# Optimization experiments

Hardware: AMD Instinct MI355X
Metric: run time of the kernel (lower is better)

The kernel has to match this reference:

```python
import jax, jax.numpy as jnp
import numpy as np

B, N, SU, H, NC, NUM_ITER = 1024, 32, 8, 64, 4, 5
E = N * (N - 1)


def _edge_idx(n):
    # Fully-connected graph without self loops; edges grouped contiguously by
    # destination node so that blocks of (n-1) messages sum into one node
    # (matches the original Python segment-sum loop with step = n-1).
    idx = np.arange(n)
    temp_a = np.concatenate([np.delete(idx, j) for j in range(n)])  # sources
    temp_b = np.repeat(idx, n - 1)                                   # destinations
    return temp_a, temp_b


def _lin(x, W, b):
    return x @ W.T + b


def setup_inputs():
    key = jax.random.key(0)
    ks = jax.random.split(key, 20)
    f = jax.random.normal
    return {
        "read_gru": f(ks[0], (B, N, SU), jnp.float32),
        "gru_init": f(ks[1], (B, N, H), jnp.float32),
        "init_features": f(ks[2], (B, N, 3), jnp.float32),
        "edge_weight": f(ks[3], (B, E), jnp.float32),
        "noise_info": jax.random.uniform(ks[4], (B, 1), jnp.float32),
        "x_hat_EP": f(ks[5], (B, N), jnp.float32),
        "variance_EP": jax.random.uniform(ks[6], (B, N), jnp.float32),
        "W1a": f(ks[7], (SU, 3)) * 0.3, "b1a": jnp.zeros((SU,)),
        "W2a": f(ks[8], (H, 2 * SU + 2)) * 0.1, "b2a": jnp.zeros((H,)),
        "W2b": f(ks[9], (H // 2, H)) * 0.1, "b2b": jnp.zeros((H // 2,)),
        "W2c": f(ks[10], (SU, H // 2)) * 0.1, "b2c": jnp.zeros((SU,)),
        "Wih": f(ks[11], (3 * H, SU + 2)) * 0.1, "bih": jnp.zeros((3 * H,)),
        "Whh": f(ks[12], (3 * H, H)) * 0.1, "bhh": jnp.zeros((3 * H,)),
        "W3a": f(ks[13], (H, SU)) * 0.1, "b3a": jnp.zeros((H,)),
        "W3b": f(ks[14], (H // 2, H)) * 0.1, "b3b": jnp.zeros((H // 2,)),
        "W3c": f(ks[15], (NC, H // 2)) * 0.1, "b3c": jnp.zeros((NC,)),
        "W4": f(ks[16], (SU, H)) * 0.1, "b4": jnp.zeros((SU,)),
        "GNN_iter": 0,
    }


def reference(read_gru, gru_init, init_features, edge_weight, noise_info,
              x_hat_EP, variance_EP,
              W1a, b1a, W2a, b2a, W2b, b2b, W2c, b2c,
              Wih, bih, Whh, bhh,
              W3a, b3a, W3b, b3b, W3c, b3c, W4, b4, GNN_iter):
    b, n = init_features.shape[0], init_features.shape[1]
    temp_a, temp_b = _edge_idx(n)
    e = temp_a.shape[0]
    edge_e = edge_weight[:, :, None]                              # [B,E,1]
    noise_e = jnp.broadcast_to(noise_info, (b, e))[:, :, None]    # [B,E,1]
    gru_hidden = gru_init
    for it in range(NUM_ITER):
        if it == 0 and GNN_iter == 0:
            init_nodes = _lin(init_features, W1a, b1a)            # [B,N,SU]
        else:
            init_nodes = read_gru
        s1 = init_nodes[:, temp_a, :]                             # gather sources
        s2 = init_nodes[:, temp_b, :]                             # gather dests
        comb = jnp.concatenate([s1, s2, edge_e, noise_e], axis=2) # [B,E,2SU+2]
        m = jax.nn.relu(_lin(comb, W2a, b2a))
        m = jax.nn.relu(_lin(m, W2b, b2b))
        m = jax.nn.relu(_lin(m, W2c, b2c))                        # [B,E,SU]
        # contiguous blocks of (n-1) messages per destination node
        sum_msgs = m.reshape(b, n, n - 1, -1).sum(axis=2)         # [B,N,SU]
        gin = jnp.concatenate(
            [sum_msgs, x_hat_EP[:, :, None], variance_EP[:, :, None]], axis=2)
        # GRUCell applied per node
        gi = _lin(gin, Wih, bih)
        gh = _lin(gru_hidden, Whh, bhh)
        i_r, i_z, i_n = jnp.split(gi, 3, axis=-1)
        h_r, h_z, h_n = jnp.split(gh, 3, axis=-1)
        r = jax.nn.sigmoid(i_r + h_r)
        z = jax.nn.sigmoid(i_z + h_z)
        cand = jnp.tanh(i_n + r * h_n)
        gru_hidden = (1.0 - z) * cand + z * gru_hidden
        read_gru = _lin(gru_hidden, W4, b4)
    # readout (no activations in original forward)
    p_y_x = _lin(_lin(_lin(read_gru, W3a, b3a), W3b, b3b), W3c, b3c)
    return (p_y_x, read_gru, gru_hidden)
```

## Files before the change

### kernel.cpp

```cpp
#include <hip/hip_runtime.h>
#include <hip/hip_bf16.h>

#define BB 1024
#define NN 32
#define SUD 8
#define HD 64
#define NCD 4
#define ED 992
#define NITER 5

#define O_W2AT 0
#define O_B2A  1152
#define O_W2B  1216
#define O_B2B  3264
#define O_W2CT 3296
#define O_B2C  3552
#define O_WIHT 3560
#define O_BIH  5480
#define O_WHHT 5672
#define O_BHH  17960
#define O_W4T  18152
#define O_B4   18664
#define O_W3AT 18672
#define O_B3A  19184
#define O_W3BT 19248
#define O_B3B  21296
#define O_W3CT 21328
#define O_B3C  21456
#define O_W1AT 21460
#define O_B1A  21484
#define W_TOTAL 21492
#define O_WIHP 21492
#define W_TOTAL2 25332

#define FRAG_B2   0
#define FRAG_C    2048
#define FRAG_WHH  2560
#define FRAG_A2P  14848
#define FRAG_TOTAL 18944
#define PREP_TOTAL (W_TOTAL2 + FRAG_TOTAL)

#define GHS 196

typedef const float* fwp;
typedef __attribute__((ext_vector_type(8))) short short8;
typedef __attribute__((ext_vector_type(4))) float float4v;
typedef __attribute__((ext_vector_type(2))) float float2v;

__device__ __forceinline__ short bf16r(float x) {
  __hip_bfloat16 h = __float2bfloat16(x);
  return __builtin_bit_cast(short, h);
}
__device__ __forceinline__ float2v mk2(float a, float b) {
  float2v r; r.x = a; r.y = b; return r;
}

__global__ void prep_weights(fwp W2a, fwp b2a, fwp W2b, fwp b2b, fwp W2c, fwp b2c,
                             fwp Wih, fwp bih, fwp Whh, fwp bhh,
                             fwp W3a, fwp b3a, fwp W3b, fwp b3b, fwp W3c, fwp b3c,
                             fwp W4, fwp b4, fwp W1a, fwp b1a, float* __restrict__ ws) {
  int idx = blockIdx.x * 256 + threadIdx.x;
  if (idx >= PREP_TOTAL) return;
  if (idx >= W_TOTAL2) {
    __hip_bfloat16* wbw = (__hip_bfloat16*)(ws + W_TOTAL2);
    int e = idx - W_TOTAL2;
    float v;
    if (e < 2048) {
      int j = e & 7, L = (e >> 3) & 63, hs = e >> 9;
      int h = hs >> 1, s = hs & 1;
      v = W2b[(2 * (L & 15) + h) * 64 + s * 32 + ((L >> 4) & 3) * 8 + j];
    } else if (e < 2560) {
      int e2 = e - 2048;
      int j = e2 & 7, L = (e2 >> 3) & 63;
      int su = L & 15, q = L >> 4;
      v = (su < 8) ? W2c[su * 32 + q * 8 + j] : 0.f;
    } else if (e < 14848) {
      int e2 = e - 2560;
      int j = e2 & 7, L = (e2 >> 3) & 63, nts = e2 >> 9;
      int nt = nts >> 1, s = nts & 1;
      v = Whh[(nt * 16 + (L & 15)) * 64 + s * 32 + ((L >> 4) & 3) * 8 + j];
    } else {
      int e2 = e - 14848;
      int j = e2 & 7, L = (e2 >> 3) & 63, nt = e2 >> 9;
      int col = L & 15, kq = L >> 4;
      v = 0.f;
      if (kq == 0) v = (nt < 4) ? W2a[(nt * 16 + col) * 18 + j]
                                : W2a[((nt - 4) * 16 + col) * 18 + 8 + j];
    }
    wbw[e] = __float2bfloat16(v);
    return;
  }
  if (idx >= W_TOTAL) {
    int p = idx - O_WIHP;
    int o = p / 20, k = (p % 20) >> 1;
    ws[idx] = Wih[o * 10 + k];
    return;
  }
  float v;
  if (idx < O_B2A)       { int p = idx;          int su = p / 64, f = p % 64;   v = W2a[f * 18 + su]; }
  else if (idx < O_W2B)  { v = b2a[idx - O_B2A]; }
  else if (idx < O_B2B)  { v = W2b[idx - O_W2B]; }
  else if (idx < O_W2CT) { v = b2b[idx - O_B2B]; }
  else if (idx < O_B2C)  { int p = idx - O_W2CT; int o = p / 8, su = p % 8;     v = W2c[su * 32 + o]; }
  else if (idx < O_WIHT) { v = b2c[idx - O_B2C]; }
  else if (idx < O_BIH)  { int p = idx - O_WIHT; int k = p / 192, o = p % 192;  v = Wih[o * 10 + k]; }
  else if (idx < O_WHHT) { v = bih[idx - O_BIH]; }
  else if (idx < O_BHH)  { int p = idx - O_WHHT; int k = p / 192, o = p % 192;  v = Whh[o * 64 + k]; }
  else if (idx < O_W4T)  { v = bhh[idx - O_BHH]; }
  else if (idx < O_B4)   { int p = idx - O_W4T;  int k = p / 8, su = p % 8;     v = W4[su * 64 + k]; }
  else if (idx < O_W3AT) { v = b4[idx - O_B4]; }
  else if (idx < O_B3A)  { int p = idx - O_W3AT; int k = p / 64, f = p % 64;    v = W3a[f * 8 + k]; }
  else if (idx < O_W3BT) { v = b3a[idx - O_B3A]; }
  else if (idx < O_B3B)  { int p = idx - O_W3BT; int k = p / 32, f = p % 32;    v = W3b[f * 64 + k]; }
  else if (idx < O_W3CT) { v = b3b[idx - O_B3B]; }
  else if (idx < O_B3C)  { int p = idx - O_W3CT; int k = p / 4, c = p % 4;      v = W3c[c * 32 + k]; }
  else if (idx < O_W1AT) { v = b3c[idx - O_B3C]; }
  else if (idx < O_B1A)  { int p = idx - O_W1AT; int c = p / 8, su = p % 8;     v = W1a[su * 3 + c]; }
  else                   { v = b1a[idx - O_B1A]; }
  ws[idx] = v;
}

#define DO_STEP2(AROW, EWV, KOFF, Y0, Y1, W0, W1, FH0, FH1, ACC0, ACC1)        \
  {                                                                            \
    float4v x0 = *(const float4v*)&sA1[(AROW) * 68 + (KOFF)];                  \
    float4v x1 = *(const float4v*)&sA1[(AROW) * 68 + (KOFF) + 4];              \
    float4v z4 = {0.f, 0.f, 0.f, 0.f};                                         \
    float4v t0 = (x0 + Y0) + (EWV) * W0;                                       \
    float4v t1 = (x1 + Y1) + (EWV) * W1;                                       \
    t0 = __builtin_elementwise_max(t0, z4);                                    \
    t1 = __builtin_elementwise_max(t1, z4);                                    \
    short8 ahi;                                                                \
    ahi[0] = bf16r(t0.x); ahi[1] = bf16r(t0.y); ahi[2] = bf16r(t0.z);          \
    ahi[3] = bf16r(t0.w); ahi[4] = bf16r(t1.x); ahi[5] = bf16r(t1.y);          \
    ahi[6] = bf16r(t1.z); ahi[7] = bf16r(t1.w);                                \
    ACC0 = __builtin_amdgcn_mfma_f32_16x16x32_bf16(ahi, FH0, ACC0, 0, 0, 0);   \
    ACC1 = __builtin_amdgcn_mfma_f32_16x16x32_bf16(ahi, FH1, ACC1, 0, 0, 0);   \
  }

#define LAUNDER(v) __asm__ __volatile__("" : "+v"(v))

__global__ __launch_bounds__(256, 4) void gnn_fused(
    const float* __restrict__ read_gru_in,
    const float* __restrict__ gru_init,
    const float* __restrict__ feat,
    const float* __restrict__ edge_w,
    const float* __restrict__ noise_in,
    const float* __restrict__ xhat,
    const float* __restrict__ vep,
    const int* __restrict__ gnn_iter_p,
    const float* __restrict__ ws,
    const float* __restrict__ W4g,
    float* __restrict__ out)
{
  __shared__ __attribute__((aligned(16))) char spool[NN * GHS * 4];
  __shared__ __attribute__((aligned(16))) float sH[NN * 68];
  __shared__ float sNodes[NN * 9];
  __shared__ float sSum[NN * 8];
  __shared__ float sEw[ED];
  __shared__ float sC1[64];
  __shared__ float sWew[64];
  __shared__ float sX[NN];
  __shared__ float sV[NN];

  float* const sA1 = (float*)spool;
  float* const sA2 = (float*)(spool + 8704);
  __hip_bfloat16* const sM2 = (__hip_bfloat16*)(spool + 17408);
  float* const sGH = (float*)spool;

  const int b = blockIdx.x;
  const int t = threadIdx.x;
  const int lane = t & 63;
  const int wv = t >> 6;
  const int quad = lane >> 4;
  const int lm = lane & 15;

  const __hip_bfloat16* wb = (const __hip_bfloat16*)(ws + W_TOTAL2);

  float noi = noise_in[b];
  for (int e = t; e < ED; e += 256) sEw[e] = edge_w[b * ED + e];
  if (t < NN) { sX[t] = xhat[b * NN + t]; sV[t] = vep[b * NN + t]; }
  if (t < 64) {
    sC1[t]  = ws[O_B2A + t] + noi * ws[O_W2AT + 17 * 64 + t];
    sWew[t] = ws[O_W2AT + 16 * 64 + t];
  }
#pragma unroll
  for (int i = 0; i < 8; ++i) {
    int p = t + 256 * i;
    sH[(p >> 6) * 68 + (p & 63)] = gru_init[b * (NN * HD) + p];
  }
  {
    const int git = gnn_iter_p[0];
    int n = t >> 3, su = t & 7;
    float acc;
    if (git == 0) {
      acc = ws[O_B1A + su];
#pragma unroll
      for (int c = 0; c < 3; ++c)
        acc += ws[O_W1AT + c * 8 + su] * feat[b * (NN * 3) + n * 3 + c];
    } else {
      acc = read_gru_in[b * (NN * SUD) + t];
    }
    sNodes[n * 9 + su] = acc;
  }
  __syncthreads();

  for (int it = 0; it < NITER; ++it) {
    int ive = 0; LAUNDER(ive);
    const float* wsle = ws + ive;
    const __hip_bfloat16* wble = wb + ive;
    short8 fbh00 = *(const short8*)(wble + FRAG_B2 + (0 * 64 + lane) * 8);
    short8 fbh01 = *(const short8*)(wble + FRAG_B2 + (1 * 64 + lane) * 8);
    short8 fbh10 = *(const short8*)(wble + FRAG_B2 + (2 * 64 + lane) * 8);
    short8 fbh11 = *(const short8*)(wble + FRAG_B2 + (3 * 64 + lane) * 8);
    short8 fcf   = *(const short8*)(wble + FRAG_C + lane * 8);
    const float2v b2bv = *(const float2v*)&wsle[O_B2B + 2 * lm];
    const float   b2cl = wsle[O_B2C + lm];

    {
      int iva = 0; LAUNDER(iva);
      const __hip_bfloat16* fp = wb + FRAG_A2P + iva;
      short8 aN[2];
#pragma unroll
      for (int mt = 0; mt < 2; ++mt) {
        short8 a = {0, 0, 0, 0, 0, 0, 0, 0};
        if (quad == 0) {
          const float* np = &sNodes[(mt * 16 + lm) * 9];
#pragma unroll
          for (int q = 0; q < 8; ++q) a[q] = bf16r(np[q]);
        }
        aN[mt] = a;
      }
      const int f = wv * 16 + lm;
      const float c1f = sC1[f];
#pragma unroll
      for (int half = 0; half < 2; ++half) {
        short8 bfr = *(const short8*)(fp + ((half * 4 + wv) * 64 + lane) * 8);
#pragma unroll
        for (int mt = 0; mt < 2; ++mt) {
          float4v acc = {0.f, 0.f, 0.f, 0.f};
          acc = __builtin_amdgcn_mfma_f32_16x16x32_bf16(aN[mt], bfr, acc, 0, 0, 0);
#pragma unroll
          for (int r = 0; r < 4; ++r) {
            int node = mt * 16 + quad * 4 + r;
            if (half == 0) sA1[node * 68 + f] = acc[r];
            else           sA2[node * 68 + f] = acc[r] + c1f;
          }
        }
      }
    }
    __syncthreads();

    {
      int ivz = 0; LAUNDER(ivz);
      __hip_bfloat16* m2w = sM2 + wv * (16 * 44);
      const int kq0 = quad * 8, kq1 = 32 + quad * 8;
      float4v wwA = *(const float4v*)&sWew[ivz + kq0];
      float4v wwB = *(const float4v*)&sWew[ivz + kq0 + 4];
      float4v wwC = *(const float4v*)&sWew[ivz + kq1];
      float4v wwD = *(const float4v*)&sWew[ivz + kq1 + 4];
      const float4v binit0 = {b2bv.x, b2bv.x, b2bv.x, b2bv.x};
      const float4v binit1 = {b2bv.y, b2bv.y, b2bv.y, b2bv.y};
      const float4v cinit  = {b2cl, b2cl, b2cl, b2cl};
      const int kkB = 16 + lm;
      const int kkB2 = (kkB < 31) ? kkB : 0;
      for (int ni = 0; ni < 8; ++ni) {
        const int jj = wv * 8 + ni;
        const int a0 = lm + (lm >= jj ? 1 : 0);
        const int a1 = kkB2 + (kkB2 >= jj ? 1 : 0);
        const float ew0 = sEw[ivz + jj * 31 + lm];
        const float ew1 = (kkB < 31) ? sEw[ivz + jj * 31 + kkB] : 0.f;
        float4v yA = *(const float4v*)&sA2[jj * 68 + kq0];
        float4v yB = *(const float4v*)&sA2[jj * 68 + kq0 + 4];
        float4v yC = *(const float4v*)&sA2[jj * 68 + kq1];
        float4v yD = *(const float4v*)&sA2[jj * 68 + kq1 + 4];
        float4v acc00 = binit0;
        float4v acc01 = binit1;
        DO_STEP2(a0, ew0, kq0, yA, yB, wwA, wwB, fbh00, fbh10, acc00, acc01);
        DO_STEP2(a0, ew0, kq1, yC, yD, wwC, wwD, fbh01, fbh11, acc00, acc01);
#pragma unroll
        for (int r = 0; r < 4; ++r) {
          float m20 = fmaxf(acc00[r], 0.f);
          float m21 = fmaxf(acc01[r], 0.f);
          ushort2 pp;
          pp.x = (unsigned short)bf16r(m20);
          pp.y = (unsigned short)bf16r(m21);
          *(ushort2*)(m2w + (quad * 4 + r) * 44 + 2 * lm) = pp;
        }
        float4v acc10 = binit0;
        float4v acc11 = binit1;
        DO_STEP2(a1, ew1, kq0, yA, yB, wwA, wwB, fbh00, fbh10, acc10, acc11);
        DO_STEP2(a1, ew1, kq1, yC, yD, wwC, wwD, fbh01, fbh11, acc10, acc11);
        __asm__ __volatile__("" ::: "memory");
        float psum;
        {
          short8 ac = *(const short8*)(m2w + lm * 44 + quad * 8);
          float4v c3 = cinit;
          c3 = __builtin_amdgcn_mfma_f32_16x16x32_bf16(ac, fcf, c3, 0, 0, 0);
          psum  = fmaxf(c3[0], 0.f);
          psum += fmaxf(c3[1], 0.f);
          psum += fmaxf(c3[2], 0.f);
          psum += fmaxf(c3[3], 0.f);
        }
        __asm__ __volatile__("" ::: "memory");
#pragma unroll
        for (int r = 0; r < 4; ++r) {
          float m20 = fmaxf(acc10[r], 0.f);
          float m21 = fmaxf(acc11[r], 0.f);
          ushort2 pp;
          pp.x = (unsigned short)bf16r(m20);
          pp.y = (unsigned short)bf16r(m21);
          *(ushort2*)(m2w + (quad * 4 + r) * 44 + 2 * lm) = pp;
        }
        __asm__ __volatile__("" ::: "memory");
        {
          short8 ac = *(const short8*)(m2w + lm * 44 + quad * 8);
          float4v c3 = cinit;
          c3 = __builtin_amdgcn_mfma_f32_16x16x32_bf16(ac, fcf, c3, 0, 0, 0);
#pragma unroll
          for (int r = 0; r < 4; ++r) {
            float v = fmaxf(c3[r], 0.f);
            if (r == 3) v = (quad == 3) ? 0.f : v;
            psum += v;
          }
        }
        __asm__ __volatile__("" ::: "memory");
        psum += __shfl_xor(psum, 16);
        psum += __shfl_xor(psum, 32);
        if (lane < 8) sSum[jj * 8 + lane] = psum;
      }
    }
    __syncthreads();

    {
      int ivg = 0; LAUNDER(ivg);
      const __hip_bfloat16* wbl = wb + ivg;
      short8 aH[2][2];
#pragma unroll
      for (int mt = 0; mt < 2; ++mt) {
#pragma unroll
        for (int s = 0; s < 2; ++s) {
          const float* hp = &sH[(mt * 16 + lm) * 68 + s * 32 + quad * 8];
          float4v h0 = *(const float4v*)hp;
          float4v h1 = *(const float4v*)(hp + 4);
          short8 a;
          a[0] = bf16r(h0.x); a[1] = bf16r(h0.y); a[2] = bf16r(h0.z); a[3] = bf16r(h0.w);
          a[4] = bf16r(h1.x); a[5] = bf16r(h1.y); a[6] = bf16r(h1.z); a[7] = bf16r(h1.w);
          aH[mt][s] = a;
        }
      }
#pragma unroll
      for (int nt = 0; nt < 3; ++nt) {
        int gnt = 4 * nt + wv;
        short8 bh0 = *(const short8*)(wbl + FRAG_WHH + ((gnt * 2 + 0) * 64 + lane) * 8);
        short8 bh1 = *(const short8*)(wbl + FRAG_WHH + ((gnt * 2 + 1) * 64 + lane) * 8);
#pragma unroll
        for (int mt = 0; mt < 2; ++mt) {
          float4v acc = {0.f, 0.f, 0.f, 0.f};
          acc = __builtin_amdgcn_mfma_f32_16x16x32_bf16(aH[mt][0], bh0, acc, 0, 0, 0);
          acc = __builtin_amdgcn_mfma_f32_16x16x32_bf16(aH[mt][1], bh1, acc, 0, 0, 0);
#pragma unroll
          for (int r = 0; r < 4; ++r)
            sGH[(mt * 16 + quad * 4 + r) * GHS + gnt * 16 + lm] = acc[r];
        }
      }
    }
    __asm__ __volatile__("" ::: "memory");

    {
      int ivq = 0; LAUNDER(ivq);
      const float* wsl = ws + ivq;
      int lm2 = lane & 15, g = lane >> 4;
      int c = wv * 16 + lm2;
      const float* wih = wsl + O_WIHP;
      float br = wsl[O_BIH + c]       + wsl[O_BHH + c];
      float bz = wsl[O_BIH + 64 + c]  + wsl[O_BHH + 64 + c];
      float bn = wsl[O_BIH + 128 + c];
      float2v ar2[4], az2[4], an2[4];
#pragma unroll
      for (int jp = 0; jp < 4; ++jp) {
        ar2[jp] = mk2(br, br); az2[jp] = mk2(bz, bz); an2[jp] = mk2(bn, bn);
      }
#pragma unroll
      for (int k = 0; k < 10; ++k) {
        float2v wr = *(const float2v*)&wih[(c) * 20 + 2 * k];
        float2v wz = *(const float2v*)&wih[(64 + c) * 20 + 2 * k];
        float2v wn = *(const float2v*)&wih[(128 + c) * 20 + 2 * k];
#pragma unroll
        for (int jp = 0; jp < 4; ++jp) {
          float2v gg;
          if (k < 8)       gg = mk2(sSum[(g + 8 * jp) * 8 + k], sSum[(g + 8 * jp + 4) * 8 + k]);
          else if (k == 8) gg = mk2(sX[g + 8 * jp], sX[g + 8 * jp + 4]);
          else             gg = mk2(sV[g + 8 * jp], sV[g + 8 * jp + 4]);
          ar2[jp] += wr * gg;
          az2[jp] += wz * gg;
          an2[jp] += wn * gg;
        }
      }
      float bnh = wsl[O_BHH + 128 + c];
      float hnew[8];
#pragma unroll
      for (int j = 0; j < 8; ++j) {
        int n = g + 4 * j;
        int jp = j >> 1;
        float arj = (j & 1) ? ar2[jp].y : ar2[jp].x;
        float azj = (j & 1) ? az2[jp].y : az2[jp].x;
        float anj = (j & 1) ? an2[jp].y : an2[jp].x;
        float ghr = sGH[n * GHS + c];
        float ghz = sGH[n * GHS + 64 + c];
        float ghn = sGH[n * GHS + 128 + c] + bnh;
        float er = __expf(-(arj + ghr));
        float r = __builtin_amdgcn_rcpf(1.f + er);
        float ez = __expf(-(azj + ghz));
        float z = __builtin_amdgcn_rcpf(1.f + ez);
        float cd = anj + r * ghn;
        float e2 = __expf(2.f * cd);
        float th = 1.f - 2.f * __builtin_amdgcn_rcpf(e2 + 1.f);
        float hv = sH[n * 68 + c];
        hnew[j] = th + z * (hv - th);
      }
      __syncthreads();
#pragma unroll
      for (int j = 0; j < 8; ++j) sH[(g + 4 * j) * 68 + c] = hnew[j];
    }
    __syncthreads();

    {
      int ivw = 0; LAUNDER(ivw);
      int n = t >> 3, su = t & 7;
      const float* w4r = W4g + ivw + su * 64;
      float4v acc4 = {0.f, 0.f, 0.f, 0.f};
#pragma unroll
      for (int k = 0; k < 64; k += 4) {
        float4v w = *(const float4v*)&w4r[k];
        float4v h = *(const float4v*)&sH[n * 68 + k];
        acc4 += w * h;
      }
      sNodes[n * 9 + su] = ws[O_B4 + su] + ((acc4.x + acc4.y) + (acc4.z + acc4.w));
    }
    __syncthreads();
  }

#pragma unroll
  for (int i = 0; i < 8; ++i) {
    int p = t + 256 * i;
    int n = p >> 6, f = p & 63;
    float acc = ws[O_B3A + f];
#pragma unroll
    for (int k = 0; k < 8; ++k) acc += ws[O_W3AT + k * 64 + f] * sNodes[n * 9 + k];
    sA1[n * 68 + f] = acc;
  }
  __syncthreads();
#pragma unroll
  for (int i = 0; i < 4; ++i) {
    int p = t + 256 * i;
    int n = p >> 5, f = p & 31;
    float c0 = 0.f, c1v = 0.f, c2 = 0.f, c3v = 0.f;
#pragma unroll
    for (int k = 0; k < 64; k += 4) {
      c0  += ws[O_W3BT + (k + 0) * 32 + f] * sA1[n * 68 + k + 0];
      c1v += ws[O_W3BT + (k + 1) * 32 + f] * sA1[n * 68 + k + 1];
      c2  += ws[O_W3BT + (k + 2) * 32 + f] * sA1[n * 68 + k + 2];
      c3v += ws[O_W3BT + (k + 3) * 32 + f] * sA1[n * 68 + k + 3];
    }
    sA2[n * 33 + f] = ws[O_B3B + f] + ((c0 + c1v) + (c2 + c3v));
  }
  __syncthreads();
  if (t < 128) {
    int n = t >> 2, c = t & 3;
    float acc = ws[O_B3C + c];
#pragma unroll
    for (int k = 0; k < 32; ++k) acc += ws[O_W3CT + k * 4 + c] * sA2[n * 33 + k];
    out[b * (NN * NCD) + t] = acc;
  }
  out[BB * NN * NCD + b * (NN * SUD) + t] = sNodes[(t >> 3) * 9 + (t & 7)];
#pragma unroll
  for (int i = 0; i < 8; ++i) {
    int p = t + 256 * i;
    out[BB * NN * NCD + BB * NN * SUD + b * (NN * HD) + p] =
        sH[(p >> 6) * 68 + (p & 63)];
  }
}

extern "C" void kernel_launch(void* const* d_in, const int* in_sizes, int n_in,
                              void* d_out, int out_size, void* d_ws, size_t ws_size,
                              hipStream_t stream) {
  typedef const float* F32;
  F32 read_gru = (F32)d_in[0];
  F32 gru_init = (F32)d_in[1];
  F32 feat     = (F32)d_in[2];
  F32 edge_w   = (F32)d_in[3];
  F32 noise    = (F32)d_in[4];
  F32 xh       = (F32)d_in[5];
  F32 vp       = (F32)d_in[6];
  F32 W1a = (F32)d_in[7];  F32 b1a = (F32)d_in[8];
  F32 W2a = (F32)d_in[9];  F32 b2a = (F32)d_in[10];
  F32 W2b = (F32)d_in[11]; F32 b2b = (F32)d_in[12];
  F32 W2c = (F32)d_in[13]; F32 b2c = (F32)d_in[14];
  F32 Wih = (F32)d_in[15]; F32 bih = (F32)d_in[16];
  F32 Whh = (F32)d_in[17]; F32 bhh = (F32)d_in[18];
  F32 W3a = (F32)d_in[19]; F32 b3a = (F32)d_in[20];
  F32 W3b = (F32)d_in[21]; F32 b3b = (F32)d_in[22];
  F32 W3c = (F32)d_in[23]; F32 b3c = (F32)d_in[24];
  F32 W4  = (F32)d_in[25]; F32 b4  = (F32)d_in[26];
  const int* git = (const int*)d_in[27];
  float* ws = (float*)d_ws;

  prep_weights<<<(PREP_TOTAL + 255) / 256, 256, 0, stream>>>(
      W2a, b2a, W2b, b2b, W2c, b2c, Wih, bih, Whh, bhh,
      W3a, b3a, W3b, b3b, W3c, b3c, W4, b4, W1a, b1a, ws);

  gnn_fused<<<BB, 256, 0, stream>>>(read_gru, gru_init, feat, edge_w, noise,
                                    xh, vp, git, ws, W4, (float*)d_out);
}
```

Measured before the change: 253.0 us.

## Fuse GRU input projection into MFMA and compute gates directly from accumulators

The GRU input-to-hidden product (summed messages, x_hat, variance against Wih) is now done with bf16 MFMA, using a new zero-padded bf16 fragment layout of Wih packed by the prep kernel. The gate nonlinearities are then applied directly to the MFMA accumulator registers, so the shared-memory round trip through the sGH buffer and its fp32 scalar FMA loop are removed. The r/z/n column split across waves is rearranged so each wave owns matching gate columns. In exchange, the input projection runs at bf16 precision instead of fp32, and the shared-memory pool is resized.

```diff
diff --git a/kernel.cpp b/kernel.cpp
--- a/kernel.cpp
+++ b/kernel.cpp
@@ -40,8 +40,6 @@
 #define FRAG_TOTAL 18944
 #define PREP_TOTAL (W_TOTAL2 + FRAG_TOTAL)
 
-#define GHS 196
-
 typedef const float* fwp;
 typedef __attribute__((ext_vector_type(8))) short short8;
 typedef __attribute__((ext_vector_type(4))) float float4v;
@@ -50,9 +48,6 @@
 __device__ __forceinline__ short bf16r(float x) {
   __hip_bfloat16 h = __float2bfloat16(x);
   return __builtin_bit_cast(short, h);
-}
-__device__ __forceinline__ float2v mk2(float a, float b) {
-  float2v r; r.x = a; r.y = b; return r;
 }
 
 __global__ void prep_weights(fwp W2a, fwp b2a, fwp W2b, fwp b2b, fwp W2c, fwp b2c,
@@ -105,7 +100,24 @@
   else if (idx < O_WIHT) { v = b2c[idx - O_B2C]; }
   else if (idx < O_BIH)  { int p = idx - O_WIHT; int k = p / 192, o = p % 192;  v = Wih[o * 10 + k]; }
   else if (idx < O_WHHT) { v = bih[idx - O_BIH]; }
-  else if (idx < O_BHH)  { int p = idx - O_WHHT; int k = p / 192, o = p % 192;  v = Whh[o * 64 + k]; }
+  else if (idx < O_BHH)  {
+    int p = idx - O_WHHT;
+    if (p < 3072) {
+      unsigned packed = 0;
+#pragma unroll
+      for (int h = 0; h < 2; ++h) {
+        int e = 2 * p + h;
+        int j = e & 7, L = (e >> 3) & 63, nt = e >> 9;
+        int k = ((L >> 4) & 3) * 8 + j;
+        float vv = (k < 10) ? Wih[(nt * 16 + (L & 15)) * 10 + k] : 0.f;
+        unsigned us = (unsigned short)bf16r(vv);
+        packed |= us << (16 * h);
+      }
+      ws[idx] = __builtin_bit_cast(float, packed);
+      return;
+    }
+    int k = p / 192, o = p % 192;  v = Whh[o * 64 + k];
+  }
   else if (idx < O_W4T)  { v = bhh[idx - O_BHH]; }
   else if (idx < O_B4)   { int p = idx - O_W4T;  int k = p / 8, su = p % 8;     v = W4[su * 64 + k]; }
   else if (idx < O_W3AT) { v = b4[idx - O_B4]; }
@@ -152,7 +164,7 @@
     const float* __restrict__ W4g,
     float* __restrict__ out)
 {
-  __shared__ __attribute__((aligned(16))) char spool[NN * GHS * 4];
+  __shared__ __attribute__((aligned(16))) char spool[23040];
   __shared__ __attribute__((aligned(16))) float sH[NN * 68];
   __shared__ float sNodes[NN * 9];
   __shared__ float sSum[NN * 8];
@@ -165,7 +177,6 @@
   float* const sA1 = (float*)spool;
   float* const sA2 = (float*)(spool + 8704);
   __hip_bfloat16* const sM2 = (__hip_bfloat16*)(spool + 17408);
-  float* const sGH = (float*)spool;
 
   const int b = blockIdx.x;
   const int t = threadIdx.x;
@@ -334,7 +345,9 @@
     {
       int ivg = 0; LAUNDER(ivg);
       const __hip_bfloat16* wbl = wb + ivg;
+      const __hip_bfloat16* wihf = (const __hip_bfloat16*)(ws + O_WHHT) + ivg;
       short8 aH[2][2];
+      short8 aG[2];
 #pragma unroll
       for (int mt = 0; mt < 2; ++mt) {
 #pragma unroll
@@ -347,80 +360,90 @@
           a[4] = bf16r(h1.x); a[5] = bf16r(h1.y); a[6] = bf16r(h1.z); a[7] = bf16r(h1.w);
           aH[mt][s] = a;
         }
-      }
-#pragma unroll
-      for (int nt = 0; nt < 3; ++nt) {
-        int gnt = 4 * nt + wv;
+        short8 g = {0, 0, 0, 0, 0, 0, 0, 0};
+        int nrow = mt * 16 + lm;
+        if (quad == 0) {
+          float4v s0 = *(const float4v*)&sSum[nrow * 8];
+          float4v s1 = *(const float4v*)&sSum[nrow * 8 + 4];
+          g[0] = bf16r(s0.x); g[1] = bf16r(s0.y); g[2] = bf16r(s0.z); g[3] = bf16r(s0.w);
+          g[4] = bf16r(s1.x); g[5] = bf16r(s1.y); g[6] = bf16r(s1.z); g[7] = bf16r(s1.w);
+        } else if (quad == 1) {
+          g[0] = bf16r(sX[nrow]);
+          g[1] = bf16r(sV[nrow]);
+        }
+        aG[mt] = g;
+      }
+      const float4v zz4 = {0.f, 0.f, 0.f, 0.f};
+      float4v pr0, pr1, pz0, pz1, phn0, phn1, pin0, pin1;
+      {
+        int gnt = wv;
         short8 bh0 = *(const short8*)(wbl + FRAG_WHH + ((gnt * 2 + 0) * 64 + lane) * 8);
         short8 bh1 = *(const short8*)(wbl + FRAG_WHH + ((gnt * 2 + 1) * 64 + lane) * 8);
-#pragma unroll
-        for (int mt = 0; mt < 2; ++mt) {
-          float4v acc = {0.f, 0.f, 0.f, 0.f};
-          acc = __builtin_amdgcn_mfma_f32_16x16x32_bf16(aH[mt][0], bh0, acc, 0, 0, 0);
-          acc = __builtin_amdgcn_mfma_f32_16x16x32_bf16(aH[mt][1], bh1, acc, 0, 0, 0);
-#pragma unroll
-          for (int r = 0; r < 4; ++r)
-            sGH[(mt * 16 + quad * 4 + r) * GHS + gnt * 16 + lm] = acc[r];
-        }
-      }
-    }
-    __asm__ __volatile__("" ::: "memory");
-
-    {
-      int ivq = 0; LAUNDER(ivq);
-      const float* wsl = ws + ivq;
-      int lm2 = lane & 15, g = lane >> 4;
-      int c = wv * 16 + lm2;
-      const float* wih = wsl + O_WIHP;
-      float br = wsl[O_BIH + c]       + wsl[O_BHH + c];
-      float bz = wsl[O_BIH + 64 + c]  + wsl[O_BHH + 64 + c];
-      float bn = wsl[O_BIH + 128 + c];
-      float2v ar2[4], az2[4], an2[4];
-#pragma unroll
-      for (int jp = 0; jp < 4; ++jp) {
-        ar2[jp] = mk2(br, br); az2[jp] = mk2(bz, bz); an2[jp] = mk2(bn, bn);
-      }
-#pragma unroll
-      for (int k = 0; k < 10; ++k) {
-        float2v wr = *(const float2v*)&wih[(c) * 20 + 2 * k];
-        float2v wz = *(const float2v*)&wih[(64 + c) * 20 + 2 * k];
-        float2v wn = *(const float2v*)&wih[(128 + c) * 20 + 2 * k];
-#pragma unroll
-        for (int jp = 0; jp < 4; ++jp) {
-          float2v gg;
-          if (k < 8)       gg = mk2(sSum[(g + 8 * jp) * 8 + k], sSum[(g + 8 * jp + 4) * 8 + k]);
-          else if (k == 8) gg = mk2(sX[g + 8 * jp], sX[g + 8 * jp + 4]);
-          else             gg = mk2(sV[g + 8 * jp], sV[g + 8 * jp + 4]);
-          ar2[jp] += wr * gg;
-          az2[jp] += wz * gg;
-          an2[jp] += wn * gg;
-        }
-      }
-      float bnh = wsl[O_BHH + 128 + c];
-      float hnew[8];
-#pragma unroll
-      for (int j = 0; j < 8; ++j) {
-        int n = g + 4 * j;
-        int jp = j >> 1;
-        float arj = (j & 1) ? ar2[jp].y : ar2[jp].x;
-        float azj = (j & 1) ? az2[jp].y : az2[jp].x;
-        float anj = (j & 1) ? an2[jp].y : an2[jp].x;
-        float ghr = sGH[n * GHS + c];
-        float ghz = sGH[n * GHS + 64 + c];
-        float ghn = sGH[n * GHS + 128 + c] + bnh;
-        float er = __expf(-(arj + ghr));
-        float r = __builtin_amdgcn_rcpf(1.f + er);
-        float ez = __expf(-(azj + ghz));
-        float z = __builtin_amdgcn_rcpf(1.f + ez);
-        float cd = anj + r * ghn;
-        float e2 = __expf(2.f * cd);
-        float th = 1.f - 2.f * __builtin_amdgcn_rcpf(e2 + 1.f);
-        float hv = sH[n * 68 + c];
-        hnew[j] = th + z * (hv - th);
+        short8 bwi = *(const short8*)(wihf + (gnt * 64 + lane) * 8);
+        pr0 = __builtin_amdgcn_mfma_f32_16x16x32_bf16(aG[0], bwi, zz4, 0, 0, 0);
+        pr0 = __builtin_amdgcn_mfma_f32_16x16x32_bf16(aH[0][0], bh0, pr0, 0, 0, 0);
+        pr0 = __builtin_amdgcn_mfma_f32_16x16x32_bf16(aH[0][1], bh1, pr0, 0, 0, 0);
+        pr1 = __builtin_amdgcn_mfma_f32_16x16x32_bf16(aG[1], bwi, zz4, 0, 0, 0);
+        pr1 = __builtin_amdgcn_mfma_f32_16x16x32_bf16(aH[1][0], bh0, pr1, 0, 0, 0);
+        pr1 = __builtin_amdgcn_mfma_f32_16x16x32_bf16(aH[1][1], bh1, pr1, 0, 0, 0);
+      }
+      {
+        int gnt = 4 + wv;
+        short8 bh0 = *(const short8*)(wbl + FRAG_WHH + ((gnt * 2 + 0) * 64 + lane) * 8);
+        short8 bh1 = *(const short8*)(wbl + FRAG_WHH + ((gnt * 2 + 1) * 64 + lane) * 8);
+        short8 bwi = *(const short8*)(wihf + (gnt * 64 + lane) * 8);
+        pz0 = __builtin_amdgcn_mfma_f32_16x16x32_bf16(aG[0], bwi, zz4, 0, 0, 0);
+        pz0 = __builtin_amdgcn_mfma_f32_16x16x32_bf16(aH[0][0], bh0, pz0, 0, 0, 0);
+        pz0 = __builtin_amdgcn_mfma_f32_16x16x32_bf16(aH[0][1], bh1, pz0, 0, 0, 0);
+        pz1 = __builtin_amdgcn_mfma_f32_16x16x32_bf16(aG[1], bwi, zz4, 0, 0, 0);
+        pz1 = __builtin_amdgcn_mfma_f32_16x16x32_bf16(aH[1][0], bh0, pz1, 0, 0, 0);
+        pz1 = __builtin_amdgcn_mfma_f32_16x16x32_bf16(aH[1][1], bh1, pz1, 0, 0, 0);
+      }
+      {
+        int gnt = 8 + wv;
+        short8 bh0 = *(const short8*)(wbl + FRAG_WHH + ((gnt * 2 + 0) * 64 + lane) * 8);
+        short8 bh1 = *(const short8*)(wbl + FRAG_WHH + ((gnt * 2 + 1) * 64 + lane) * 8);
+        short8 bwi = *(const short8*)(wihf + (gnt * 64 + lane) * 8);
+        phn0 = __builtin_amdgcn_mfma_f32_16x16x32_bf16(aH[0][0], bh0, zz4, 0, 0, 0);
+        phn0 = __builtin_amdgcn_mfma_f32_16x16x32_bf16(aH[0][1], bh1, phn0, 0, 0, 0);
+        phn1 = __builtin_amdgcn_mfma_f32_16x16x32_bf16(aH[1][0], bh0, zz4, 0, 0, 0);
+        phn1 = __builtin_amdgcn_mfma_f32_16x16x32_bf16(aH[1][1], bh1, phn1, 0, 0, 0);
+        pin0 = __builtin_amdgcn_mfma_f32_16x16x32_bf16(aG[0], bwi, zz4, 0, 0, 0);
+        pin1 = __builtin_amdgcn_mfma_f32_16x16x32_bf16(aG[1], bwi, zz4, 0, 0, 0);
+      }
+      const int c = wv * 16 + lm;
+      const float br  = ws[O_BIH + c]       + ws[O_BHH + c];
+      const float bz  = ws[O_BIH + 64 + c]  + ws[O_BHH + 64 + c];
+      const float bni = ws[O_BIH + 128 + c];
+      const float bnh = ws[O_BHH + 128 + c];
+      float4v hn0, hn1;
+#pragma unroll
+      for (int mt = 0; mt < 2; ++mt) {
+#pragma unroll
+        for (int rr = 0; rr < 4; ++rr) {
+          int n = mt * 16 + quad * 4 + rr;
+          float pre_r = ((mt == 0) ? pr0[rr]  : pr1[rr])  + br;
+          float pre_z = ((mt == 0) ? pz0[rr]  : pz1[rr])  + bz;
+          float i_n   = ((mt == 0) ? pin0[rr] : pin1[rr]) + bni;
+          float h_n   = ((mt == 0) ? phn0[rr] : phn1[rr]) + bnh;
+          float er = __expf(-pre_r);
+          float r = __builtin_amdgcn_rcpf(1.f + er);
+          float ez = __expf(-pre_z);
+          float z = __builtin_amdgcn_rcpf(1.f + ez);
+          float cd = i_n + r * h_n;
+          float e2 = __expf(2.f * cd);
+          float th = 1.f - 2.f * __builtin_amdgcn_rcpf(e2 + 1.f);
+          float hv = sH[n * 68 + c];
+          float hnew = th + z * (hv - th);
+          if (mt == 0) hn0[rr] = hnew; else hn1[rr] = hnew;
+        }
       }
       __syncthreads();
 #pragma unroll
-      for (int j = 0; j < 8; ++j) sH[(g + 4 * j) * 68 + c] = hnew[j];
+      for (int rr = 0; rr < 4; ++rr) {
+        sH[(quad * 4 + rr) * 68 + c]      = hn0[rr];
+        sH[(16 + quad * 4 + rr) * 68 + c] = hn1[rr];
+      }
     }
     __syncthreads();
 
```

Measured after the change: 245.5 us, median of 2. 2.9% less time.
